# Kernel optimization log

Hardware: AMD Instinct MI355X
Metric: run time of the kernel (lower is better)

Reference implementation:

```python
import jax, jax.numpy as jnp
import numpy as np

N, H, HEADS, SLICES = 200000, 256, 8, 64
DH = H // HEADS  # 32


def setup_inputs() -> dict:
    key = jax.random.key(0)
    ks = jax.random.split(key, 13)
    r = lambda k, shape, scale: jax.random.normal(k, shape, dtype=jnp.float32) * scale
    return {
        "x": r(ks[0], (N, H), 1.0),
        "Wx": r(ks[1], (H, H), H ** -0.5),
        "bx": r(ks[2], (H,), 0.02),
        "Wfx": r(ks[3], (H, H), H ** -0.5),
        "bfx": r(ks[4], (H,), 0.02),
        "Wslice": r(ks[5], (SLICES, DH), DH ** -0.5),
        "bslice": r(ks[6], (SLICES,), 0.02),
        "Wq": r(ks[7], (DH, DH), DH ** -0.5),
        "Wk": r(ks[8], (DH, DH), DH ** -0.5),
        "Wv": r(ks[9], (DH, DH), DH ** -0.5),
        "Wout": r(ks[10], (H, H), H ** -0.5),
        "bout": r(ks[11], (H,), 0.02),
        "temperature": jnp.full((HEADS, 1, 1), 0.5, dtype=jnp.float32),
    }


def reference(x, Wx, bx, Wfx, bfx, Wslice, bslice, Wq, Wk, Wv, Wout, bout, temperature):
    n, hidden = x.shape
    heads, dh = HEADS, DH
    scale = dh ** -0.5

    def to_heads(y):  # (n, hidden) -> (heads, n, dh)
        return jnp.transpose(y.reshape(n, heads, dh), (1, 0, 2))

    fx_mid = to_heads(x @ Wfx.T + bfx)              # (h, n, d)
    x_mid = to_heads(x @ Wx.T + bx)                 # (h, n, d)

    temp = jnp.clip(temperature, 0.1, 5.0)          # (h, 1, 1)
    slice_logits = (jnp.einsum('hnd,gd->hng', x_mid, Wslice) + bslice) / temp
    slice_weights = jax.nn.softmax(slice_logits, axis=-1)   # (h, n, g)
    slice_norm = jnp.sum(slice_weights, axis=1)              # (h, g)

    slice_token = jnp.einsum('hnc,hng->hgc', fx_mid, slice_weights)
    slice_token = slice_token / (slice_norm[:, :, None] + 1e-05)  # (h, g, d)

    q = jnp.einsum('hgd,ed->hge', slice_token, Wq)
    k = jnp.einsum('hgd,ed->hge', slice_token, Wk)
    v = jnp.einsum('hgd,ed->hge', slice_token, Wv)

    dots = jnp.einsum('hgd,hkd->hgk', q, k) * scale
    attn = jax.nn.softmax(dots, axis=-1)
    out_slice = jnp.einsum('hgk,hkd->hgd', attn, v)          # (h, g, d)

    out_x = jnp.einsum('hgc,hng->hnc', out_slice, slice_weights)  # (h, n, d)
    out_x = jnp.transpose(out_x, (1, 0, 2)).reshape(n, hidden)
    return out_x @ Wout.T + bout
```

## Files before the change

kernel.cpp:

```cpp
#include <hip/hip_runtime.h>

typedef unsigned short u16;
typedef __attribute__((ext_vector_type(2))) unsigned int u32x2;
typedef __attribute__((ext_vector_type(4))) unsigned int u32x4;
typedef __attribute__((ext_vector_type(4))) float f32x4;
typedef __attribute__((ext_vector_type(8))) short bf16x8;

__device__ __forceinline__ float bf2f(u16 u) {
    union { unsigned int i; float f; } v; v.i = ((unsigned int)u) << 16; return v.f;
}
__device__ __forceinline__ u16 f2bf(float f) {
    union { float f; unsigned int i; } v; v.f = f;
    unsigned int x = v.i;
    return (u16)((x + 0x7fffu + ((x >> 16) & 1u)) >> 16);
}
__device__ __forceinline__ unsigned int pack2(float a, float b) {
    return (unsigned int)f2bf(a) | ((unsigned int)f2bf(b) << 16);
}
__device__ __forceinline__ void split2(float a, float b, unsigned int& h, unsigned int& l) {
    u16 ha = f2bf(a), hb = f2bf(b);
    u16 la = f2bf(a - bf2f(ha)), lb = f2bf(b - bf2f(hb));
    h = (unsigned int)ha | ((unsigned int)hb << 16);
    l = (unsigned int)la | ((unsigned int)lb << 16);
}

__device__ __forceinline__ f32x4 MFMA(bf16x8 a, bf16x8 b, f32x4 c) {
    return __builtin_amdgcn_mfma_f32_16x16x32_bf16(a, b, c, 0, 0, 0);
}

__global__ __launch_bounds__(256) void kprep(
    const float* __restrict__ Wx, const float* __restrict__ bx,
    const float* __restrict__ Wfx, const float* __restrict__ Wslice,
    const float* __restrict__ bslice, const float* __restrict__ temperature,
    u16* __restrict__ Wcomb, float* __restrict__ bcomb, u16* __restrict__ WfxT)
{
    const int gidx = blockIdx.x * 256 + threadIdx.x;
    if (gidx < 131072) {
        const int hg = gidx >> 8, k = gidx & 255;
        const int h = hg >> 6, g = hg & 63;
        float tc = fminf(fmaxf(temperature[h], 0.1f), 5.0f);
        const float invt = 1.0f / tc;
        float s = 0.f;
        #pragma unroll
        for (int d = 0; d < 32; ++d) s += Wslice[g * 32 + d] * Wx[(h * 32 + d) * 256 + k];
        Wcomb[hg * 256 + k] = f2bf(s * invt);
    } else if (gidx < 131072 + 65536) {
        const int i = gidx - 131072;
        WfxT[i] = f2bf(Wfx[i]);
    } else if (gidx < 131072 + 65536 + 512) {
        const int hg = gidx - 131072 - 65536;
        const int h = hg >> 6, g = hg & 63;
        float tc = fminf(fmaxf(temperature[h], 0.1f), 5.0f);
        float s = bslice[g];
        #pragma unroll
        for (int d = 0; d < 32; ++d) s += Wslice[g * 32 + d] * bx[h * 32 + d];
        bcomb[hg] = s / tc;
    }
}

#define LDS_XH 98304
#define LDS_XL 131072
__global__ __launch_bounds__(512, 2) void kAB(
    const float* __restrict__ x, const u16* __restrict__ Wcomb,
    const float* __restrict__ bcomb, const u16* __restrict__ WfxT,
    const float* __restrict__ bfx,
    u16* __restrict__ swg, float* __restrict__ pst, float* __restrict__ pnorm)
{
    __shared__ char lds[163840];
    const int tid  = threadIdx.x;
    const int wv   = tid >> 6;
    const int lane = tid & 63;
    const int l15  = lane & 15;
    const int l4   = lane >> 4;
    const int hl   = wv >> 2;
    const int tq   = wv & 3;

    const int bid = blockIdx.x;
    const int c   = bid >> 2;
    const int hp  = bid & 3;
    const int head = hp * 2 + hl;

    for (int u = tid; u < 6144; u += 512) {
        const int row = u >> 5, seg = u & 31;
        const u16* src = (row < 128)
            ? Wcomb + ((size_t)hp * 128 + row) * 256 + seg * 8
            : WfxT  + ((size_t)hp * 64 + (row - 128)) * 256 + seg * 8;
        u32x4 v = *(const u32x4*)src;
        *(u32x4*)(lds + ((row * 512 + seg * 16) ^ ((row & 7) << 4))) = v;
    }

    float bc[4], bfv[2];
    #pragma unroll
    for (int fc = 0; fc < 4; ++fc) bc[fc] = bcomb[head * 64 + fc * 16 + l15];
    #pragma unroll
    for (int fc = 0; fc < 2; ++fc) bfv[fc] = bfx[head * 32 + fc * 16 + l15];

    f32x4 stacc[2][4];
    #pragma unroll
    for (int i = 0; i < 2; ++i)
        #pragma unroll
        for (int j = 0; j < 4; ++j) stacc[i][j] = (f32x4){0.f, 0.f, 0.f, 0.f};
    float nacc[4] = {0.f, 0.f, 0.f, 0.f};

    const int cnt = 12 + (c < 53 ? 1 : 0);
    const long tb = (long)c * 12 + (c < 53 ? c : 53);

    const int row = tid >> 3, seg = tid & 7;
    const int xswz = (row & 7) << 4;

    f32x4 pf[8];
    #pragma unroll
    for (int i = 0; i < 8; ++i)
        pf[i] = *(const f32x4*)(x + (size_t)(tb * 64 + row) * 256 + i * 32 + seg * 4);

    const int xrow  = tq * 16 + l15;
    const int xoff  = xrow * 512;
    const int xkey  = (xrow & 7) << 4;
    const int bwrow0 = hl * 64 + l15;
    const int bfrow0 = 128 + hl * 32 + l15;

    for (int t = 0; t < cnt; ++t) {
        const long tok0 = (tb + t) * 64;

        __syncthreads();
        #pragma unroll
        for (int i = 0; i < 8; ++i) {
            unsigned int h0, l0, h1, l1;
            split2(pf[i][0], pf[i][1], h0, l0);
            split2(pf[i][2], pf[i][3], h1, l1);
            const int a = (row * 512 + i * 64 + seg * 8) ^ xswz;
            *(u32x2*)(lds + LDS_XH + a) = (u32x2){h0, h1};
            *(u32x2*)(lds + LDS_XL + a) = (u32x2){l0, l1};
        }
        __syncthreads();

        f32x4 accF[2], accL[4];
        #pragma unroll
        for (int fc = 0; fc < 2; ++fc) accF[fc] = (f32x4){bfv[fc], bfv[fc], bfv[fc], bfv[fc]};
        #pragma unroll
        for (int fc = 0; fc < 4; ++fc) accL[fc] = (f32x4){bc[fc], bc[fc], bc[fc], bc[fc]};
        #pragma unroll
        for (int ks = 0; ks < 8; ++ks) {
            const int kb = ks * 64 + l4 * 16;
            bf16x8 ah = *(const bf16x8*)(lds + LDS_XH + ((xoff + kb) ^ xkey));
            bf16x8 al = *(const bf16x8*)(lds + LDS_XL + ((xoff + kb) ^ xkey));
            bf16x8 bw[4], bfF[2];
            #pragma unroll
            for (int fc = 0; fc < 4; ++fc) {
                const int r2 = bwrow0 + fc * 16;
                bw[fc] = *(const bf16x8*)(lds + ((r2 * 512 + kb) ^ ((r2 & 7) << 4)));
            }
            #pragma unroll
            for (int fc = 0; fc < 2; ++fc) {
                const int r2 = bfrow0 + fc * 16;
                bfF[fc] = *(const bf16x8*)(lds + ((r2 * 512 + kb) ^ ((r2 & 7) << 4)));
            }
            #pragma unroll
            for (int fc = 0; fc < 2; ++fc) accF[fc] = MFMA(ah, bfF[fc], accF[fc]);
            #pragma unroll
            for (int fc = 0; fc < 4; ++fc) {
                accL[fc] = MFMA(ah, bw[fc], accL[fc]);
                accL[fc] = MFMA(al, bw[fc], accL[fc]);
            }
        }

        if (t + 1 < cnt) {
            #pragma unroll
            for (int i = 0; i < 8; ++i)
                pf[i] = *(const f32x4*)(x + (size_t)(tok0 + 64 + row) * 256 + i * 32 + seg * 4);
        }

        float mrow[4], srow4[4];
        #pragma unroll
        for (int r = 0; r < 4; ++r)
            mrow[r] = fmaxf(fmaxf(accL[0][r], accL[1][r]), fmaxf(accL[2][r], accL[3][r]));
        #pragma unroll
        for (int d = 1; d <= 8; d <<= 1)
            #pragma unroll
            for (int r = 0; r < 4; ++r)
                mrow[r] = fmaxf(mrow[r], __shfl_xor(mrow[r], d));
        #pragma unroll
        for (int r = 0; r < 4; ++r) {
            float e0 = __expf(accL[0][r] - mrow[r]);
            float e1 = __expf(accL[1][r] - mrow[r]);
            float e2 = __expf(accL[2][r] - mrow[r]);
            float e3 = __expf(accL[3][r] - mrow[r]);
            accL[0][r] = e0; accL[1][r] = e1; accL[2][r] = e2; accL[3][r] = e3;
            srow4[r] = e0 + e1 + e2 + e3;
        }
        #pragma unroll
        for (int d = 1; d <= 8; d <<= 1)
            #pragma unroll
            for (int r = 0; r < 4; ++r)
                srow4[r] += __shfl_xor(srow4[r], d);
        #pragma unroll
        for (int r = 0; r < 4; ++r) {
            const float inv = 1.0f / srow4[r];
            float e0 = accL[0][r] * inv, e1 = accL[1][r] * inv;
            float e2 = accL[2][r] * inv, e3 = accL[3][r] * inv;
            accL[0][r] = e0; accL[1][r] = e1; accL[2][r] = e2; accL[3][r] = e3;
            nacc[0] += e0; nacc[1] += e1; nacc[2] += e2; nacc[3] += e3;
        }

        __syncthreads();

        unsigned int pL[4][2];
        #pragma unroll
        for (int fc = 0; fc < 4; ++fc) {
            u16 w0 = f2bf(accL[fc][0]), w1 = f2bf(accL[fc][1]);
            u16 w2 = f2bf(accL[fc][2]), w3 = f2bf(accL[fc][3]);
            pL[fc][0] = (unsigned int)w0 | ((unsigned int)w1 << 16);
            pL[fc][1] = (unsigned int)w2 | ((unsigned int)w3 << 16);
            const int col2 = (hl * 64 + fc * 16 + l15) * 2;
            #pragma unroll
            for (int r = 0; r < 4; ++r) {
                const int tok = tq * 16 + l4 * 4 + r;
                const u16 val = (r == 0) ? w0 : (r == 1) ? w1 : (r == 2) ? w2 : w3;
                *(u16*)(lds + LDS_XL + ((tok * 256 + col2) ^ ((tok & 7) << 4))) = val;
            }
        }

        unsigned int pF[2][2];
        #pragma unroll
        for (int fc = 0; fc < 2; ++fc) {
            pF[fc][0] = pack2(accF[fc][0], accF[fc][1]);
            pF[fc][1] = pack2(accF[fc][2], accF[fc][3]);
        }
        #pragma unroll
        for (int mt2 = 0; mt2 < 2; ++mt2) {
            union { u32x4 u; bf16x8 b; } a;
            a.u = (u32x4){pF[mt2][0], pF[mt2][1], 0u, 0u};
            #pragma unroll
            for (int nt = 0; nt < 4; ++nt) {
                union { u32x4 u; bf16x8 b; } bb;
                bb.u = (u32x4){pL[nt][0], pL[nt][1], 0u, 0u};
                stacc[mt2][nt] = MFMA(a.b, bb.b, stacc[mt2][nt]);
            }
        }

        __syncthreads();

        #pragma unroll
        for (int q = 0; q < 2; ++q) {
            const int slot = tid * 2 + q;
            const int tok = slot >> 4, sg = slot & 15;
            u32x4 v = *(const u32x4*)(lds + LDS_XL + ((tok * 256 + sg * 16) ^ ((tok & 7) << 4)));
            __builtin_nontemporal_store(v,
                (u32x4*)(swg + (size_t)(tok0 + tok) * 512 + hp * 128 + sg * 8));
        }
    }

    __syncthreads();
    float* sst = (float*)(lds + LDS_XH);
    float* nst = (float*)lds;
    #pragma unroll
    for (int mt2 = 0; mt2 < 2; ++mt2)
        #pragma unroll
        for (int nt = 0; nt < 4; ++nt)
            #pragma unroll
            for (int r = 0; r < 4; ++r)
                sst[wv * 2048 + (mt2 * 16 + l4 * 4 + r) * 64 + nt * 16 + l15] = stacc[mt2][nt][r];
    #pragma unroll
    for (int fc = 0; fc < 4; ++fc) {
        float v = nacc[fc];
        v += __shfl_xor(v, 16); v += __shfl_xor(v, 32);
        if (l4 == 0) nst[wv * 64 + fc * 16 + l15] = v;
    }
    __syncthreads();
    for (int i = tid; i < 4096; i += 512) {
        const int hl2 = i >> 11, e = i & 2047;
        float s = sst[(hl2 * 4 + 0) * 2048 + e] + sst[(hl2 * 4 + 1) * 2048 + e]
                + sst[(hl2 * 4 + 2) * 2048 + e] + sst[(hl2 * 4 + 3) * 2048 + e];
        __builtin_nontemporal_store(s,
            pst + ((size_t)(hp * 2 + hl2) * 256 + c) * 2048 + e);
    }
    if (tid < 128) {
        const int hl2 = tid >> 6, g = tid & 63;
        float s = nst[(hl2 * 4 + 0) * 64 + g] + nst[(hl2 * 4 + 1) * 64 + g]
                + nst[(hl2 * 4 + 2) * 64 + g] + nst[(hl2 * 4 + 3) * 64 + g];
        pnorm[((size_t)(hp * 2 + hl2) * 256 + c) * 64 + g] = s;
    }
}

__global__ __launch_bounds__(256) void kC1(
    const float* __restrict__ pst, const float* __restrict__ pnorm,
    float* __restrict__ stn, float* __restrict__ norm)
{
    __shared__ float red[256];
    const int tid  = threadIdx.x;
    const int half = tid >> 7;
    const int li   = tid & 127;
    if (blockIdx.x < 128) {
        const int o  = blockIdx.x * 128 + li;
        const int h  = o >> 11, oo = o & 2047;
        float s = 0.f;
        for (int b = half * 128; b < half * 128 + 128; ++b)
            s += __builtin_nontemporal_load(pst + ((size_t)h * 256 + b) * 2048 + oo);
        red[tid] = s;
        __syncthreads();
        if (!half) stn[o] = red[li] + red[li + 128];
    } else {
        const int o = (blockIdx.x - 128) * 128 + li;
        const int h = o >> 6, g = o & 63;
        float s = 0.f;
        for (int b = half * 128; b < half * 128 + 128; ++b)
            s += pnorm[((size_t)h * 256 + b) * 64 + g];
        red[tid] = s;
        __syncthreads();
        if (!half) norm[o] = red[li] + red[li + 128];
    }
}

__global__ __launch_bounds__(64) void kattn(
    const float* __restrict__ stn, const float* __restrict__ norm,
    const float* __restrict__ Wq, const float* __restrict__ Wk,
    const float* __restrict__ Wv, float* __restrict__ os)
{
    __shared__ float kl[2048], vl[2048];
    const int h = blockIdx.x, g = threadIdx.x;
    const float ng = norm[h * 64 + g] + 1e-5f;
    float s[32];
    #pragma unroll
    for (int d = 0; d < 32; ++d) s[d] = stn[h * 2048 + d * 64 + g] / ng;
    float q[32];
    #pragma unroll
    for (int e = 0; e < 32; ++e) {
        float aq = 0.f, ak = 0.f, av = 0.f;
        #pragma unroll
        for (int d = 0; d < 32; ++d) {
            aq += s[d] * Wq[e * 32 + d];
            ak += s[d] * Wk[e * 32 + d];
            av += s[d] * Wv[e * 32 + d];
        }
        q[e] = aq; kl[g * 32 + e] = ak; vl[g * 32 + e] = av;
    }
    __syncthreads();
    float p[64];
    float mx = -1e30f;
    const float scale = 0.17677669529663689f;
    #pragma unroll
    for (int kk = 0; kk < 64; ++kk) {
        float a = 0.f;
        #pragma unroll
        for (int e = 0; e < 32; ++e) a += q[e] * kl[kk * 32 + e];
        a *= scale; p[kk] = a; mx = fmaxf(mx, a);
    }
    float sum = 0.f;
    #pragma unroll
    for (int kk = 0; kk < 64; ++kk) { p[kk] = __expf(p[kk] - mx); sum += p[kk]; }
    const float inv = 1.0f / sum;
    #pragma unroll
    for (int d = 0; d < 32; ++d) {
        float a = 0.f;
        #pragma unroll
        for (int kk = 0; kk < 64; ++kk) a += p[kk] * inv * vl[kk * 32 + d];
        os[h * 2048 + g * 32 + d] = a;
    }
}

__global__ __launch_bounds__(64) void kD2(
    const float* __restrict__ os, const float* __restrict__ Wout,
    u16* __restrict__ Wc2T)
{
    const int co = blockIdx.x;
    for (int rep = 0; rep < 8; ++rep) {
        const int hg = rep * 64 + threadIdx.x;
        const int h = hg >> 6, g = hg & 63;
        float s = 0.f;
        #pragma unroll
        for (int d = 0; d < 32; ++d)
            s += os[h * 2048 + g * 32 + d] * Wout[co * 256 + h * 32 + d];
        Wc2T[co * 512 + hg] = f2bf(s);
    }
}

__global__ __launch_bounds__(512, 1) void kE(
    const u16* __restrict__ swg, const u16* __restrict__ Wc2T,
    const float* __restrict__ bout, float* __restrict__ y)
{
    __shared__ char lds[131072];
    const int tid  = threadIdx.x;
    const int w    = tid >> 6;
    const int lane = tid & 63;
    const int l15  = lane & 15;
    const int l4   = lane >> 4;
    const int aswz = (l15 & 7) << 4;

    const int bid = blockIdx.x;
    const int cnt = 12 + (bid < 53 ? 1 : 0);
    const long tb = (long)bid * 12 + (bid < 53 ? bid : 53);

    bf16x8 Breg[16][2];
    #pragma unroll
    for (int ks = 0; ks < 16; ++ks)
        #pragma unroll
        for (int fc = 0; fc < 2; ++fc)
            Breg[ks][fc] = *(const bf16x8*)(Wc2T +
                (size_t)(w * 32 + fc * 16 + l15) * 512 + ks * 32 + l4 * 8);

    const float b0 = bout[w * 32 + l15], b1 = bout[w * 32 + 16 + l15];

    const int row = tid >> 3, seg = tid & 7;
    const int sbase = row * 1024 + seg * 128;
    const int sswz  = (row & 7) << 4;

    u32x4 pf[8];
    {
        const u32x4* sp = (const u32x4*)(swg + (size_t)(tb * 64 + row) * 512 + seg * 64);
        #pragma unroll
        for (int c = 0; c < 8; ++c) pf[c] = __builtin_nontemporal_load(sp + c);
    }

    for (int t = 0; t < cnt; ++t) {
        const long tok0 = (tb + t) * 64;
        char* buf = lds + ((t & 1) << 16);

        #pragma unroll
        for (int c = 0; c < 8; ++c)
            *(u32x4*)(buf + ((sbase + c * 16) ^ sswz)) = pf[c];
        __syncthreads();

        if (t + 1 < cnt) {
            const u32x4* sp = (const u32x4*)(swg + (size_t)(tok0 + 64 + row) * 512 + seg * 64);
            #pragma unroll
            for (int c = 0; c < 8; ++c) pf[c] = __builtin_nontemporal_load(sp + c);
        }

        f32x4 acc[4][2];
        #pragma unroll
        for (int mt = 0; mt < 4; ++mt) {
            acc[mt][0] = (f32x4){b0, b0, b0, b0};
            acc[mt][1] = (f32x4){b1, b1, b1, b1};
        }

        #pragma unroll
        for (int ks = 0; ks < 16; ++ks) {
            bf16x8 a[4];
            #pragma unroll
            for (int mt = 0; mt < 4; ++mt)
                a[mt] = *(const bf16x8*)(buf + (mt * 16 + l15) * 1024 + ((ks * 64 + l4 * 16) ^ aswz));
            #pragma unroll
            for (int mt = 0; mt < 4; ++mt)
                #pragma unroll
                for (int fc = 0; fc < 2; ++fc)
                    acc[mt][fc] = MFMA(a[mt], Breg[ks][fc], acc[mt][fc]);
        }

        #pragma unroll
        for (int mt = 0; mt < 4; ++mt)
            #pragma unroll
            for (int fc = 0; fc < 2; ++fc)
                #pragma unroll
                for (int r = 0; r < 4; ++r) {
                    const long n = tok0 + mt * 16 + l4 * 4 + r;
                    __builtin_nontemporal_store(acc[mt][fc][r],
                        y + (size_t)n * 256 + w * 32 + fc * 16 + l15);
                }
    }
}

extern "C" void kernel_launch(void* const* d_in, const int* in_sizes, int n_in,
                              void* d_out, int out_size, void* d_ws, size_t ws_size,
                              hipStream_t stream) {
    const float* x       = (const float*)d_in[0];
    const float* Wx      = (const float*)d_in[1];
    const float* bx      = (const float*)d_in[2];
    const float* Wfx     = (const float*)d_in[3];
    const float* bfx     = (const float*)d_in[4];
    const float* Wslice  = (const float*)d_in[5];
    const float* bslice  = (const float*)d_in[6];
    const float* Wq      = (const float*)d_in[7];
    const float* Wk      = (const float*)d_in[8];
    const float* Wv      = (const float*)d_in[9];
    const float* Wout    = (const float*)d_in[10];
    const float* bout    = (const float*)d_in[11];
    const float* temp    = (const float*)d_in[12];

    char* wsb = (char*)d_ws;
    u16*   sw    = (u16*)(wsb);
    float* pst   = (float*)(wsb + 204800000);
    float* pnorm = (float*)(wsb + 238354432);
    u16*   Wcomb = (u16*)(wsb + 239403008);
    float* bcomb = (float*)(wsb + 239665152);
    u16*   WfxT  = (u16*)(wsb + 239667200);
    u16*   Wc2T  = (u16*)(wsb + 239798272);
    float* os    = (float*)(wsb + 240060416);
    float* stn   = (float*)(wsb + 240125952);
    float* norm  = (float*)(wsb + 240191488);
    float* y     = (float*)d_out;

    kprep<<<770, 256, 0, stream>>>(Wx, bx, Wfx, Wslice, bslice, temp, Wcomb, bcomb, WfxT);
    kAB<<<1024, 512, 0, stream>>>(x, Wcomb, bcomb, WfxT, bfx, sw, pst, pnorm);
    kC1<<<132, 256, 0, stream>>>(pst, pnorm, stn, norm);
    kattn<<<8, 64, 0, stream>>>(stn, norm, Wq, Wk, Wv, os);
    kD2<<<256, 64, 0, stream>>>(os, Wout, Wc2T);
    kE<<<256, 512, 0, stream>>>(sw, Wc2T, bout, y);
}
```

Before: 648.3 us.

## Unfold slice projection into two-stage MFMA with register-resident x and lighter kE

kAB no longer uses the precombined Wslice·Wx weight. It computes x_mid per head with split-bf16 MFMAs and then applies Wslice as a second small MFMA stage. x tiles are now converted to hi/lo bf16 directly in registers, so they are no longer staged through LDS. This halves kAB's LDS footprint and cuts the number of x-times-weight MFMAs. kE now streams B fragments from global memory instead of holding them in registers, uses a single LDS buffer, runs twice as many blocks, and targets higher occupancy. The risks are extra global/L2 traffic for the B operand and an odd 1.0019 scale applied to the fx accumulator, which may change precision.

```diff
diff --git a/kernel.cpp b/kernel.cpp
--- a/kernel.cpp
+++ b/kernel.cpp
@@ -17,11 +17,14 @@
 __device__ __forceinline__ unsigned int pack2(float a, float b) {
     return (unsigned int)f2bf(a) | ((unsigned int)f2bf(b) << 16);
 }
-__device__ __forceinline__ void split2(float a, float b, unsigned int& h, unsigned int& l) {
-    u16 ha = f2bf(a), hb = f2bf(b);
-    u16 la = f2bf(a - bf2f(ha)), lb = f2bf(b - bf2f(hb));
-    h = (unsigned int)ha | ((unsigned int)hb << 16);
-    l = (unsigned int)la | ((unsigned int)lb << 16);
+__device__ __forceinline__ void tsplit2(float a, float b,
+                                        unsigned int& h, unsigned int& l) {
+    unsigned int ua = __float_as_uint(a), ub = __float_as_uint(b);
+    float fa = __uint_as_float(ua & 0xffff0000u);
+    float fb = __uint_as_float(ub & 0xffff0000u);
+    h = (ua >> 16) | (ub & 0xffff0000u);
+    float la = a - fa, lb = b - fb;
+    l = (__float_as_uint(la) >> 16) | (__float_as_uint(lb) & 0xffff0000u);
 }
 
 __device__ __forceinline__ f32x4 MFMA(bf16x8 a, bf16x8 b, f32x4 c) {
@@ -29,44 +32,45 @@
 }
 
 __global__ __launch_bounds__(256) void kprep(
-    const float* __restrict__ Wx, const float* __restrict__ bx,
-    const float* __restrict__ Wfx, const float* __restrict__ Wslice,
-    const float* __restrict__ bslice, const float* __restrict__ temperature,
-    u16* __restrict__ Wcomb, float* __restrict__ bcomb, u16* __restrict__ WfxT)
+    const float* __restrict__ Wx, const float* __restrict__ Wfx,
+    const float* __restrict__ Wslice, const float* __restrict__ bslice,
+    const float* __restrict__ temperature,
+    u16* __restrict__ WxTb, u16* __restrict__ WfxTg,
+    u16* __restrict__ WsP, float* __restrict__ bslv)
 {
     const int gidx = blockIdx.x * 256 + threadIdx.x;
-    if (gidx < 131072) {
-        const int hg = gidx >> 8, k = gidx & 255;
-        const int h = hg >> 6, g = hg & 63;
+    if (gidx < 65536) {
+        WxTb[gidx] = f2bf(Wx[gidx]);
+    } else if (gidx < 131072) {
+        const int i = gidx - 65536;
+        WfxTg[i] = f2bf(Wfx[i]);
+    } else if (gidx < 147456) {
+        const int i = gidx - 131072;
+        const int h = i >> 11;
+        const int rem = i & 2047;
+        const int gfc = rem >> 9;
+        const int l = (rem >> 3) & 63;
+        const int j = i & 7;
+        const int g = gfc * 16 + (l & 15);
+        const int d = ((j >> 2) << 4) + ((l >> 4) << 2) + (j & 3);
         float tc = fminf(fmaxf(temperature[h], 0.1f), 5.0f);
-        const float invt = 1.0f / tc;
-        float s = 0.f;
-        #pragma unroll
-        for (int d = 0; d < 32; ++d) s += Wslice[g * 32 + d] * Wx[(h * 32 + d) * 256 + k];
-        Wcomb[hg * 256 + k] = f2bf(s * invt);
-    } else if (gidx < 131072 + 65536) {
-        const int i = gidx - 131072;
-        WfxT[i] = f2bf(Wfx[i]);
-    } else if (gidx < 131072 + 65536 + 512) {
-        const int hg = gidx - 131072 - 65536;
-        const int h = hg >> 6, g = hg & 63;
+        WsP[i] = f2bf(Wslice[g * 32 + d] / tc);
+    } else if (gidx < 147968) {
+        const int i = gidx - 147456;
+        const int h = i >> 6, g = i & 63;
         float tc = fminf(fmaxf(temperature[h], 0.1f), 5.0f);
-        float s = bslice[g];
-        #pragma unroll
-        for (int d = 0; d < 32; ++d) s += Wslice[g * 32 + d] * bx[h * 32 + d];
-        bcomb[hg] = s / tc;
-    }
-}
-
-#define LDS_XH 98304
-#define LDS_XL 131072
+        bslv[i] = bslice[g] / tc;
+    }
+}
+
 __global__ __launch_bounds__(512, 2) void kAB(
-    const float* __restrict__ x, const u16* __restrict__ Wcomb,
-    const float* __restrict__ bcomb, const u16* __restrict__ WfxT,
-    const float* __restrict__ bfx,
+    const float* __restrict__ x, const u16* __restrict__ WxTb,
+    const u16* __restrict__ WfxTg, const u16* __restrict__ WsP,
+    const float* __restrict__ bx, const float* __restrict__ bfx,
+    const float* __restrict__ bslv,
     u16* __restrict__ swg, float* __restrict__ pst, float* __restrict__ pnorm)
 {
-    __shared__ char lds[163840];
+    __shared__ char lds[81920];
     const int tid  = threadIdx.x;
     const int wv   = tid >> 6;
     const int lane = tid & 63;
@@ -75,25 +79,37 @@
     const int hl   = wv >> 2;
     const int tq   = wv & 3;
 
-    const int bid = blockIdx.x;
-    const int c   = bid >> 2;
-    const int hp  = bid & 3;
+    const int bid  = blockIdx.x;
+    const int c    = bid >> 2;
+    const int hp   = bid & 3;
     const int head = hp * 2 + hl;
 
-    for (int u = tid; u < 6144; u += 512) {
+    for (int u = tid; u < 4096; u += 512) {
         const int row = u >> 5, seg = u & 31;
-        const u16* src = (row < 128)
-            ? Wcomb + ((size_t)hp * 128 + row) * 256 + seg * 8
-            : WfxT  + ((size_t)hp * 64 + (row - 128)) * 256 + seg * 8;
-        u32x4 v = *(const u32x4*)src;
-        *(u32x4*)(lds + ((row * 512 + seg * 16) ^ ((row & 7) << 4))) = v;
-    }
-
-    float bc[4], bfv[2];
-    #pragma unroll
-    for (int fc = 0; fc < 4; ++fc) bc[fc] = bcomb[head * 64 + fc * 16 + l15];
+        const u16* src;
+        if (row < 64)
+            src = WxTb + ((size_t)(hp * 2 + (row >> 5)) * 32 + (row & 31)) * 256 + seg * 8;
+        else {
+            const int rr = row - 64;
+            src = WfxTg + ((size_t)(hp * 2 + (rr >> 5)) * 32 + (rr & 31)) * 256 + seg * 8;
+        }
+        *(u32x4*)(lds + ((row * 512 + seg * 16) ^ ((row & 7) << 4))) = *(const u32x4*)src;
+    }
+
+    bf16x8 wsp[4];
+    #pragma unroll
+    for (int g = 0; g < 4; ++g)
+        wsp[g] = *(const bf16x8*)(WsP + (size_t)head * 2048 + g * 512 + lane * 8);
+    float bsl[4], bfv[2], bxv[2][4];
+    #pragma unroll
+    for (int g = 0; g < 4; ++g) bsl[g] = bslv[head * 64 + g * 16 + l15];
     #pragma unroll
     for (int fc = 0; fc < 2; ++fc) bfv[fc] = bfx[head * 32 + fc * 16 + l15];
+    #pragma unroll
+    for (int fc = 0; fc < 2; ++fc)
+        #pragma unroll
+        for (int r = 0; r < 4; ++r)
+            bxv[fc][r] = bx[head * 32 + fc * 16 + l4 * 4 + r];
 
     f32x4 stacc[2][4];
     #pragma unroll
@@ -105,69 +121,96 @@
     const int cnt = 12 + (c < 53 ? 1 : 0);
     const long tb = (long)c * 12 + (c < 53 ? c : 53);
 
-    const int row = tid >> 3, seg = tid & 7;
-    const int xswz = (row & 7) << 4;
-
-    f32x4 pf[8];
-    #pragma unroll
-    for (int i = 0; i < 8; ++i)
-        pf[i] = *(const f32x4*)(x + (size_t)(tb * 64 + row) * 256 + i * 32 + seg * 4);
-
-    const int xrow  = tq * 16 + l15;
-    const int xoff  = xrow * 512;
-    const int xkey  = (xrow & 7) << 4;
-    const int bwrow0 = hl * 64 + l15;
-    const int bfrow0 = 128 + hl * 32 + l15;
+    const int rowoff = (tq * 16 + l15) * 256 + l4 * 8;
+
+    f32x4 pf[16];
+    {
+        const float* xp = x + (size_t)(tb * 64) * 256 + rowoff;
+        #pragma unroll
+        for (int ks = 0; ks < 8; ++ks) {
+            pf[2 * ks]     = *(const f32x4*)(xp + ks * 32);
+            pf[2 * ks + 1] = *(const f32x4*)(xp + ks * 32 + 4);
+        }
+    }
+    __syncthreads();
 
     for (int t = 0; t < cnt; ++t) {
         const long tok0 = (tb + t) * 64;
 
-        __syncthreads();
-        #pragma unroll
-        for (int i = 0; i < 8; ++i) {
-            unsigned int h0, l0, h1, l1;
-            split2(pf[i][0], pf[i][1], h0, l0);
-            split2(pf[i][2], pf[i][3], h1, l1);
-            const int a = (row * 512 + i * 64 + seg * 8) ^ xswz;
-            *(u32x2*)(lds + LDS_XH + a) = (u32x2){h0, h1};
-            *(u32x2*)(lds + LDS_XL + a) = (u32x2){l0, l1};
-        }
-        __syncthreads();
-
-        f32x4 accF[2], accL[4];
-        #pragma unroll
-        for (int fc = 0; fc < 2; ++fc) accF[fc] = (f32x4){bfv[fc], bfv[fc], bfv[fc], bfv[fc]};
-        #pragma unroll
-        for (int fc = 0; fc < 4; ++fc) accL[fc] = (f32x4){bc[fc], bc[fc], bc[fc], bc[fc]};
+        f32x4 acc1[2], accF[2];
+        #pragma unroll
+        for (int fc = 0; fc < 2; ++fc) {
+            acc1[fc] = (f32x4){0.f, 0.f, 0.f, 0.f};
+            accF[fc] = (f32x4){0.f, 0.f, 0.f, 0.f};
+        }
         #pragma unroll
         for (int ks = 0; ks < 8; ++ks) {
+            union { u32x4 u; bf16x8 b; } bh, bl;
+            {
+                f32x4 p0 = pf[2 * ks], p1 = pf[2 * ks + 1];
+                unsigned int h0, l0, h1, l1, h2, l2, h3, l3;
+                tsplit2(p0[0], p0[1], h0, l0);
+                tsplit2(p0[2], p0[3], h1, l1);
+                tsplit2(p1[0], p1[1], h2, l2);
+                tsplit2(p1[2], p1[3], h3, l3);
+                bh.u = (u32x4){h0, h1, h2, h3};
+                bl.u = (u32x4){l0, l1, l2, l3};
+            }
             const int kb = ks * 64 + l4 * 16;
-            bf16x8 ah = *(const bf16x8*)(lds + LDS_XH + ((xoff + kb) ^ xkey));
-            bf16x8 al = *(const bf16x8*)(lds + LDS_XL + ((xoff + kb) ^ xkey));
-            bf16x8 bw[4], bfF[2];
-            #pragma unroll
-            for (int fc = 0; fc < 4; ++fc) {
-                const int r2 = bwrow0 + fc * 16;
-                bw[fc] = *(const bf16x8*)(lds + ((r2 * 512 + kb) ^ ((r2 & 7) << 4)));
-            }
+            bf16x8 awx[2], awf[2];
             #pragma unroll
             for (int fc = 0; fc < 2; ++fc) {
-                const int r2 = bfrow0 + fc * 16;
-                bfF[fc] = *(const bf16x8*)(lds + ((r2 * 512 + kb) ^ ((r2 & 7) << 4)));
-            }
-            #pragma unroll
-            for (int fc = 0; fc < 2; ++fc) accF[fc] = MFMA(ah, bfF[fc], accF[fc]);
-            #pragma unroll
-            for (int fc = 0; fc < 4; ++fc) {
-                accL[fc] = MFMA(ah, bw[fc], accL[fc]);
-                accL[fc] = MFMA(al, bw[fc], accL[fc]);
-            }
+                const int r1 = hl * 32 + fc * 16 + l15;
+                awx[fc] = *(const bf16x8*)(lds + ((r1 * 512 + kb) ^ ((r1 & 7) << 4)));
+                const int r2 = 64 + hl * 32 + fc * 16 + l15;
+                awf[fc] = *(const bf16x8*)(lds + ((r2 * 512 + kb) ^ ((r2 & 7) << 4)));
+            }
+            #pragma unroll
+            for (int fc = 0; fc < 2; ++fc) {
+                accF[fc] = MFMA(bh.b, awf[fc], accF[fc]);
+                acc1[fc] = MFMA(awx[fc], bh.b, acc1[fc]);
+                acc1[fc] = MFMA(awx[fc], bl.b, acc1[fc]);
+            }
+        }
+        #pragma unroll
+        for (int fc = 0; fc < 2; ++fc)
+            #pragma unroll
+            for (int r = 0; r < 4; ++r)
+                accF[fc][r] = accF[fc][r] * 1.001953125f + bfv[fc];
+
+        union { u32x4 u; bf16x8 b; } a2h, a2l;
+        {
+            unsigned int ah0, al0, ah1, al1, ah2, al2, ah3, al3;
+            float m0 = acc1[0][0] + bxv[0][0];
+            float m1 = acc1[0][1] + bxv[0][1];
+            float m2 = acc1[0][2] + bxv[0][2];
+            float m3 = acc1[0][3] + bxv[0][3];
+            tsplit2(m0, m1, ah0, al0);
+            tsplit2(m2, m3, ah1, al1);
+            float n0 = acc1[1][0] + bxv[1][0];
+            float n1 = acc1[1][1] + bxv[1][1];
+            float n2 = acc1[1][2] + bxv[1][2];
+            float n3 = acc1[1][3] + bxv[1][3];
+            tsplit2(n0, n1, ah2, al2);
+            tsplit2(n2, n3, ah3, al3);
+            a2h.u = (u32x4){ah0, ah1, ah2, ah3};
+            a2l.u = (u32x4){al0, al1, al2, al3};
+        }
+        f32x4 accL[4];
+        #pragma unroll
+        for (int g = 0; g < 4; ++g) {
+            accL[g] = (f32x4){bsl[g], bsl[g], bsl[g], bsl[g]};
+            accL[g] = MFMA(a2h.b, wsp[g], accL[g]);
+            accL[g] = MFMA(a2l.b, wsp[g], accL[g]);
         }
 
         if (t + 1 < cnt) {
-            #pragma unroll
-            for (int i = 0; i < 8; ++i)
-                pf[i] = *(const f32x4*)(x + (size_t)(tok0 + 64 + row) * 256 + i * 32 + seg * 4);
+            const float* xn = x + (size_t)(tok0 + 64) * 256 + rowoff;
+            #pragma unroll
+            for (int ks = 0; ks < 8; ++ks) {
+                pf[2 * ks]     = *(const f32x4*)(xn + ks * 32);
+                pf[2 * ks + 1] = *(const f32x4*)(xn + ks * 32 + 4);
+            }
         }
 
         float mrow[4], srow4[4];
@@ -216,7 +259,7 @@
             for (int r = 0; r < 4; ++r) {
                 const int tok = tq * 16 + l4 * 4 + r;
                 const u16 val = (r == 0) ? w0 : (r == 1) ? w1 : (r == 2) ? w2 : w3;
-                *(u16*)(lds + LDS_XL + ((tok * 256 + col2) ^ ((tok & 7) << 4))) = val;
+                *(u16*)(lds + 65536 + ((tok * 256 + col2) ^ ((tok & 7) << 4))) = val;
             }
         }
 
@@ -244,15 +287,15 @@
         for (int q = 0; q < 2; ++q) {
             const int slot = tid * 2 + q;
             const int tok = slot >> 4, sg = slot & 15;
-            u32x4 v = *(const u32x4*)(lds + LDS_XL + ((tok * 256 + sg * 16) ^ ((tok & 7) << 4)));
+            u32x4 v = *(const u32x4*)(lds + 65536 + ((tok * 256 + sg * 16) ^ ((tok & 7) << 4)));
             __builtin_nontemporal_store(v,
                 (u32x4*)(swg + (size_t)(tok0 + tok) * 512 + hp * 128 + sg * 8));
         }
     }
 
     __syncthreads();
-    float* sst = (float*)(lds + LDS_XH);
-    float* nst = (float*)lds;
+    float* sst = (float*)lds;
+    float* nst = (float*)(lds + 65536);
     #pragma unroll
     for (int mt2 = 0; mt2 < 2; ++mt2)
         #pragma unroll
@@ -374,11 +417,11 @@
     }
 }
 
-__global__ __launch_bounds__(512, 1) void kE(
+__global__ __launch_bounds__(512, 4) void kE(
     const u16* __restrict__ swg, const u16* __restrict__ Wc2T,
     const float* __restrict__ bout, float* __restrict__ y)
 {
-    __shared__ char lds[131072];
+    __shared__ char lds[65536];
     const int tid  = threadIdx.x;
     const int w    = tid >> 6;
     const int lane = tid & 63;
@@ -387,17 +430,10 @@
     const int aswz = (l15 & 7) << 4;
 
     const int bid = blockIdx.x;
-    const int cnt = 12 + (bid < 53 ? 1 : 0);
-    const long tb = (long)bid * 12 + (bid < 53 ? bid : 53);
-
-    bf16x8 Breg[16][2];
-    #pragma unroll
-    for (int ks = 0; ks < 16; ++ks)
-        #pragma unroll
-        for (int fc = 0; fc < 2; ++fc)
-            Breg[ks][fc] = *(const bf16x8*)(Wc2T +
-                (size_t)(w * 32 + fc * 16 + l15) * 512 + ks * 32 + l4 * 8);
-
+    const int cnt = 6 + (bid < 53 ? 1 : 0);
+    const long tb = (long)bid * 6 + (bid < 53 ? bid : 53);
+
+    const u16* Bp = Wc2T + (size_t)(w * 32 + l15) * 512 + l4 * 8;
     const float b0 = bout[w * 32 + l15], b1 = bout[w * 32 + 16 + l15];
 
     const int row = tid >> 3, seg = tid & 7;
@@ -413,11 +449,10 @@
 
     for (int t = 0; t < cnt; ++t) {
         const long tok0 = (tb + t) * 64;
-        char* buf = lds + ((t & 1) << 16);
 
         #pragma unroll
         for (int c = 0; c < 8; ++c)
-            *(u32x4*)(buf + ((sbase + c * 16) ^ sswz)) = pf[c];
+            *(u32x4*)(lds + ((sbase + c * 16) ^ sswz)) = pf[c];
         __syncthreads();
 
         if (t + 1 < cnt) {
@@ -435,15 +470,17 @@
 
         #pragma unroll
         for (int ks = 0; ks < 16; ++ks) {
+            bf16x8 bf0 = *(const bf16x8*)(Bp + ks * 32);
+            bf16x8 bf1 = *(const bf16x8*)(Bp + (size_t)16 * 512 + ks * 32);
             bf16x8 a[4];
             #pragma unroll
             for (int mt = 0; mt < 4; ++mt)
-                a[mt] = *(const bf16x8*)(buf + (mt * 16 + l15) * 1024 + ((ks * 64 + l4 * 16) ^ aswz));
-            #pragma unroll
-            for (int mt = 0; mt < 4; ++mt)
-                #pragma unroll
-                for (int fc = 0; fc < 2; ++fc)
-                    acc[mt][fc] = MFMA(a[mt], Breg[ks][fc], acc[mt][fc]);
+                a[mt] = *(const bf16x8*)(lds + (mt * 16 + l15) * 1024 + ((ks * 64 + l4 * 16) ^ aswz));
+            #pragma unroll
+            for (int mt = 0; mt < 4; ++mt) {
+                acc[mt][0] = MFMA(a[mt], bf0, acc[mt][0]);
+                acc[mt][1] = MFMA(a[mt], bf1, acc[mt][1]);
+            }
         }
 
         #pragma unroll
@@ -456,6 +493,7 @@
                     __builtin_nontemporal_store(acc[mt][fc][r],
                         y + (size_t)n * 256 + w * 32 + fc * 16 + l15);
                 }
+        __syncthreads();
     }
 }
 
@@ -480,19 +518,20 @@
     u16*   sw    = (u16*)(wsb);
     float* pst   = (float*)(wsb + 204800000);
     float* pnorm = (float*)(wsb + 238354432);
-    u16*   Wcomb = (u16*)(wsb + 239403008);
-    float* bcomb = (float*)(wsb + 239665152);
-    u16*   WfxT  = (u16*)(wsb + 239667200);
+    u16*   WxTb  = (u16*)(wsb + 239403008);
+    u16*   WfxTg = (u16*)(wsb + 239534080);
+    u16*   WsP   = (u16*)(wsb + 239665152);
+    float* bslv  = (float*)(wsb + 239697920);
     u16*   Wc2T  = (u16*)(wsb + 239798272);
     float* os    = (float*)(wsb + 240060416);
     float* stn   = (float*)(wsb + 240125952);
     float* norm  = (float*)(wsb + 240191488);
     float* y     = (float*)d_out;
 
-    kprep<<<770, 256, 0, stream>>>(Wx, bx, Wfx, Wslice, bslice, temp, Wcomb, bcomb, WfxT);
-    kAB<<<1024, 512, 0, stream>>>(x, Wcomb, bcomb, WfxT, bfx, sw, pst, pnorm);
+    kprep<<<578, 256, 0, stream>>>(Wx, Wfx, Wslice, bslice, temp, WxTb, WfxTg, WsP, bslv);
+    kAB<<<1024, 512, 0, stream>>>(x, WxTb, WfxTg, WsP, bx, bfx, bslv, sw, pst, pnorm);
     kC1<<<132, 256, 0, stream>>>(pst, pnorm, stn, norm);
     kattn<<<8, 64, 0, stream>>>(stn, norm, Wq, Wk, Wv, os);
     kD2<<<256, 64, 0, stream>>>(os, Wout, Wc2T);
-    kE<<<256, 512, 0, stream>>>(sw, Wc2T, bout, y);
-}
+    kE<<<512, 512, 0, stream>>>(sw, Wc2T, bout, y);
+}
```

Result: slower. 975.4 us (+50.4%).

## Halve kE token tile, run two blocks per CU, stage output via LDS

Applied to the files above, without the earlier changes.

kE now handles 32-token tiles instead of 64, launches 512 blocks, and sets launch bounds to two blocks per CU. LDS drops to 64 KB so two blocks can fit, and the double-buffered input is replaced by a single buffer. The output accumulators are now transposed through LDS and written as coalesced 16-byte row stores instead of scattered 4-byte stores. The aim is more latency hiding and better write efficiency on the memory-bound output. The cost is a tighter per-thread register budget with the 128-register B fragments held in registers, which risks spills, plus an extra barrier per tile.

```diff
diff --git a/kernel.cpp b/kernel.cpp
--- a/kernel.cpp
+++ b/kernel.cpp
@@ -374,11 +374,11 @@
     }
 }
 
-__global__ __launch_bounds__(512, 1) void kE(
+__global__ __launch_bounds__(512, 2) void kE(
     const u16* __restrict__ swg, const u16* __restrict__ Wc2T,
     const float* __restrict__ bout, float* __restrict__ y)
 {
-    __shared__ char lds[131072];
+    __shared__ char lds[65536];
     const int tid  = threadIdx.x;
     const int w    = tid >> 6;
     const int lane = tid & 63;
@@ -387,8 +387,8 @@
     const int aswz = (l15 & 7) << 4;
 
     const int bid = blockIdx.x;
-    const int cnt = 12 + (bid < 53 ? 1 : 0);
-    const long tb = (long)bid * 12 + (bid < 53 ? bid : 53);
+    const int cnt = 12 + (bid < 106 ? 1 : 0);
+    const long tb = (long)bid * 12 + (bid < 106 ? bid : 106);
 
     bf16x8 Breg[16][2];
     #pragma unroll
@@ -400,62 +400,77 @@
 
     const float b0 = bout[w * 32 + l15], b1 = bout[w * 32 + 16 + l15];
 
-    const int row = tid >> 3, seg = tid & 7;
-    const int sbase = row * 1024 + seg * 128;
-    const int sswz  = (row & 7) << 4;
-
-    u32x4 pf[8];
-    {
-        const u32x4* sp = (const u32x4*)(swg + (size_t)(tb * 64 + row) * 512 + seg * 64);
-        #pragma unroll
-        for (int c = 0; c < 8; ++c) pf[c] = __builtin_nontemporal_load(sp + c);
+    u32x4 pf[4];
+    #pragma unroll
+    for (int k = 0; k < 4; ++k) {
+        const int slot = tid + k * 512;
+        const int srow = slot >> 6, ss = slot & 63;
+        pf[k] = __builtin_nontemporal_load(
+            (const u32x4*)(swg + (size_t)(tb * 32 + srow) * 512 + ss * 8));
     }
 
     for (int t = 0; t < cnt; ++t) {
-        const long tok0 = (tb + t) * 64;
-        char* buf = lds + ((t & 1) << 16);
-
-        #pragma unroll
-        for (int c = 0; c < 8; ++c)
-            *(u32x4*)(buf + ((sbase + c * 16) ^ sswz)) = pf[c];
+        const long tok0 = (tb + t) * 32;
+
+        #pragma unroll
+        for (int k = 0; k < 4; ++k) {
+            const int slot = tid + k * 512;
+            const int srow = slot >> 6, ss = slot & 63;
+            *(u32x4*)(lds + ((srow * 1024 + ss * 16) ^ ((srow & 7) << 4))) = pf[k];
+        }
         __syncthreads();
 
         if (t + 1 < cnt) {
-            const u32x4* sp = (const u32x4*)(swg + (size_t)(tok0 + 64 + row) * 512 + seg * 64);
-            #pragma unroll
-            for (int c = 0; c < 8; ++c) pf[c] = __builtin_nontemporal_load(sp + c);
-        }
-
-        f32x4 acc[4][2];
-        #pragma unroll
-        for (int mt = 0; mt < 4; ++mt) {
+            #pragma unroll
+            for (int k = 0; k < 4; ++k) {
+                const int slot = tid + k * 512;
+                const int srow = slot >> 6, ss = slot & 63;
+                pf[k] = __builtin_nontemporal_load(
+                    (const u32x4*)(swg + (size_t)(tok0 + 32 + srow) * 512 + ss * 8));
+            }
+        }
+
+        f32x4 acc[2][2];
+        #pragma unroll
+        for (int mt = 0; mt < 2; ++mt) {
             acc[mt][0] = (f32x4){b0, b0, b0, b0};
             acc[mt][1] = (f32x4){b1, b1, b1, b1};
         }
 
         #pragma unroll
         for (int ks = 0; ks < 16; ++ks) {
-            bf16x8 a[4];
-            #pragma unroll
-            for (int mt = 0; mt < 4; ++mt)
-                a[mt] = *(const bf16x8*)(buf + (mt * 16 + l15) * 1024 + ((ks * 64 + l4 * 16) ^ aswz));
-            #pragma unroll
-            for (int mt = 0; mt < 4; ++mt)
-                #pragma unroll
-                for (int fc = 0; fc < 2; ++fc)
-                    acc[mt][fc] = MFMA(a[mt], Breg[ks][fc], acc[mt][fc]);
-        }
-
-        #pragma unroll
-        for (int mt = 0; mt < 4; ++mt)
+            bf16x8 a[2];
+            #pragma unroll
+            for (int mt = 0; mt < 2; ++mt)
+                a[mt] = *(const bf16x8*)(lds + (mt * 16 + l15) * 1024 + ((ks * 64 + l4 * 16) ^ aswz));
+            #pragma unroll
+            for (int mt = 0; mt < 2; ++mt) {
+                acc[mt][0] = MFMA(a[mt], Breg[ks][0], acc[mt][0]);
+                acc[mt][1] = MFMA(a[mt], Breg[ks][1], acc[mt][1]);
+            }
+        }
+
+        #pragma unroll
+        for (int mt = 0; mt < 2; ++mt)
             #pragma unroll
             for (int fc = 0; fc < 2; ++fc)
                 #pragma unroll
                 for (int r = 0; r < 4; ++r) {
-                    const long n = tok0 + mt * 16 + l4 * 4 + r;
-                    __builtin_nontemporal_store(acc[mt][fc][r],
-                        y + (size_t)n * 256 + w * 32 + fc * 16 + l15);
+                    const int tok = mt * 16 + l4 * 4 + r;
+                    const int col = w * 32 + fc * 16 + l15;
+                    *(float*)(lds + 32768 + ((tok * 1024 + col * 4) ^ ((tok & 7) << 4))) =
+                        acc[mt][fc][r];
                 }
+        __syncthreads();
+
+        #pragma unroll
+        for (int k = 0; k < 4; ++k) {
+            const int slot = tid + k * 512;
+            const int yrow = slot >> 6, ys = slot & 63;
+            u32x4 v = *(const u32x4*)(lds + 32768 + ((yrow * 1024 + ys * 16) ^ ((yrow & 7) << 4)));
+            __builtin_nontemporal_store(v,
+                (u32x4*)(y + (size_t)(tok0 + yrow) * 256 + ys * 4));
+        }
     }
 }
 
@@ -494,5 +509,5 @@
     kC1<<<132, 256, 0, stream>>>(pst, pnorm, stn, norm);
     kattn<<<8, 64, 0, stream>>>(stn, norm, Wq, Wk, Wv, os);
     kD2<<<256, 64, 0, stream>>>(os, Wout, Wc2T);
-    kE<<<256, 512, 0, stream>>>(sw, Wc2T, bout, y);
-}
+    kE<<<512, 512, 0, stream>>>(sw, Wc2T, bout, y);
+}
```

Measured after the change: 563.5 us. 1.15x faster.
